# Kernel tuning notes

Hardware: AMD Instinct MI355X
Metric: run time of the kernel (lower is better)

Reference implementation:

```python
import jax, jax.numpy as jnp
import numpy as np

N_SLOW = 26
N_FAST = 12


def _ema(x, N):
    # x: [B, T, F]; standard EMA with alpha = 2/(N+1), initialized y_0 = x_0.
    alpha = jnp.asarray(2.0 / (N + 1), dtype=x.dtype)
    one_m = jnp.asarray(1.0, dtype=x.dtype) - alpha
    xt = jnp.moveaxis(x, 1, 0)  # [T, B, F] for scan over time

    def step(carry, xi):
        y = alpha * xi + one_m * carry
        return y, y

    y0 = xt[0]
    _, ys = jax.lax.scan(step, y0, xt[1:])
    ys = jnp.concatenate([y0[None], ys], axis=0)  # [T, B, F]
    return jnp.moveaxis(ys, 0, 1)  # [B, T, F]


def setup_inputs() -> dict:
    key = jax.random.key(0)
    x = jax.random.normal(key, (4096, 2048, 8), dtype=jnp.float32)
    return {"x": x}


def reference(x):
    # MACD_RNN.forward: EMA_slow(x) - EMA_fast(x)
    return _ema(x, N_SLOW) - _ema(x, N_FAST)
```

## Files before the change

kernel.cpp:

```cpp
#include <hip/hip_runtime.h>


#define T_LEN 2048
#define FDIM 8
#define CHUNK 4
#define NTHR 512
#define NWAVE (NTHR / 64)
#define NF4 (T_LEN * FDIM / 4)
#define SLOTS_PER_CHUNK (CHUNK * FDIM / 4)

__device__ __forceinline__ float pow4(float v) {
    float v2 = v * v;
    return v2 * v2;
}

__device__ __forceinline__ int swz(int g) { return g ^ ((g >> 4) & 7); }

__global__ __launch_bounds__(NTHR, 4)
void macd_kernel(const float* __restrict__ x, float* __restrict__ out) {
    const float AS  = (float)(2.0 / 27.0);
    const float AF  = (float)(2.0 / 13.0);
    const float OMS = 1.0f - AS;
    const float OMF = 1.0f - AF;
    const float DS  = pow4(OMS);
    const float DF  = pow4(OMF);

    __shared__ float4 xb4[NF4];
    __shared__ float  W[NWAVE][16];

    const int b = blockIdx.x;
    const int j = threadIdx.x;
    const int w = j >> 6;
    const int l = j & 63;

    const float4* xg = reinterpret_cast<const float4*>(x   + (size_t)b * T_LEN * FDIM);
    float4*       og = reinterpret_cast<float4*>      (out + (size_t)b * T_LEN * FDIM);

#pragma unroll
    for (int k = 0; k < NF4 / NTHR; ++k) {
        int g = k * NTHR + j;
        xb4[swz(g)] = xg[g];
    }
    __syncthreads();

    const int c   = j;
    const int base = SLOTS_PER_CHUNK * c;
    const int key  = (c >> 1) & 7;
    float p[16];
#pragma unroll
    for (int s = 0; s < 16; ++s) p[s] = 0.f;

#pragma unroll
    for (int t = 0; t < CHUNK; ++t) {
        float4 lo = xb4[base + ((2 * t    ) ^ key)];
        float4 hi = xb4[base + ((2 * t + 1) ^ key)];
        float xx[FDIM] = {lo.x, lo.y, lo.z, lo.w, hi.x, hi.y, hi.z, hi.w};
#pragma unroll
        for (int f = 0; f < FDIM; ++f) {
            p[2 * f + 0] = AS * xx[f] + OMS * p[2 * f + 0];
            p[2 * f + 1] = AF * xx[f] + OMF * p[2 * f + 1];
        }
    }

    const float* xs = reinterpret_cast<const float*>(xb4);
    if (j == 0) {
#pragma unroll
        for (int f = 0; f < FDIM; ++f) {
            float x0 = xs[f];
            p[2 * f + 0] += DS * x0;
            p[2 * f + 1] += DF * x0;
        }
    }

    float Ms = DS, Mf = DF;
#pragma unroll
    for (int off = 1; off < 64; off <<= 1) {
#pragma unroll
        for (int s = 0; s < 16; ++s) {
            float tv = __shfl_up(p[s], (unsigned)off, 64);
            if (l >= off) p[s] += ((s & 1) ? Mf : Ms) * tv;
        }
        Ms *= Ms; Mf *= Mf;
    }

    float qe[16];
#pragma unroll
    for (int s = 0; s < 16; ++s) qe[s] = __shfl_up(p[s], 1u, 64);

    if (l == 63) {
#pragma unroll
        for (int s = 0; s < 16; ++s) W[w][s] = p[s];
    }
    __syncthreads();

    float Sp[16];
#pragma unroll
    for (int s = 0; s < 16; ++s) Sp[s] = 0.f;
    for (int v = 0; v < w; ++v) {
#pragma unroll
        for (int s = 0; s < 16; ++s)
            Sp[s] = W[v][s] + ((s & 1) ? Mf : Ms) * Sp[s];
    }

    float Dls = 1.f, Dlf = 1.f, ms2 = DS, mf2 = DF;
#pragma unroll
    for (int bit = 0; bit < 6; ++bit) {
        if ((l >> bit) & 1) { Dls *= ms2; Dlf *= mf2; }
        ms2 *= ms2; mf2 *= mf2;
    }

    float ys[FDIM], yf[FDIM];
#pragma unroll
    for (int f = 0; f < FDIM; ++f) {
        float cs = (l == 0) ? Sp[2 * f + 0] : qe[2 * f + 0] + Dls * Sp[2 * f + 0];
        float cf = (l == 0) ? Sp[2 * f + 1] : qe[2 * f + 1] + Dlf * Sp[2 * f + 1];
        ys[f] = cs; yf[f] = cf;
    }
    if (j == 0) {
#pragma unroll
        for (int f = 0; f < FDIM; ++f) { ys[f] = xs[f]; yf[f] = xs[f]; }
    }

#pragma unroll
    for (int t = 0; t < CHUNK; ++t) {
        int slo = base + ((2 * t    ) ^ key);
        int shi = base + ((2 * t + 1) ^ key);
        float4 lo = xb4[slo];
        float4 hi = xb4[shi];
        float xx[FDIM] = {lo.x, lo.y, lo.z, lo.w, hi.x, hi.y, hi.z, hi.w};
        float o[FDIM];
#pragma unroll
        for (int f = 0; f < FDIM; ++f) {
            ys[f] = AS * xx[f] + OMS * ys[f];
            yf[f] = AF * xx[f] + OMF * yf[f];
            o[f] = ys[f] - yf[f];
        }
        float4 olo = {o[0], o[1], o[2], o[3]};
        float4 ohi = {o[4], o[5], o[6], o[7]};
        xb4[slo] = olo;
        xb4[shi] = ohi;
    }
    __syncthreads();

#pragma unroll
    for (int k = 0; k < NF4 / NTHR; ++k) {
        int g = k * NTHR + j;
        og[g] = xb4[swz(g)];
    }
}

extern "C" void kernel_launch(void* const* d_in, const int* in_sizes, int n_in,
                              void* d_out, int out_size, void* d_ws, size_t ws_size,
                              hipStream_t stream) {
    (void)n_in; (void)d_ws; (void)ws_size; (void)out_size;
    const float* x = (const float*)d_in[0];
    float* out = (float*)d_out;
    const int B = in_sizes[0] / (T_LEN * FDIM);
    macd_kernel<<<dim3(B), dim3(NTHR), 0, stream>>>(x, out);
}
```

Before: 110.7 us.

## Use persistent blocks with register prefetch and double-buffered LDS

```diff
diff --git a/kernel.cpp b/kernel.cpp
--- a/kernel.cpp
+++ b/kernel.cpp
@@ -2,150 +2,166 @@
 
 
 #define T_LEN 2048
-#define FDIM 8
+#define FDIM  8
 #define CHUNK 4
-#define NTHR 512
+#define NTHR  512
 #define NWAVE (NTHR / 64)
-#define NF4 (T_LEN * FDIM / 4)
-#define SLOTS_PER_CHUNK (CHUNK * FDIM / 4)
-
-__device__ __forceinline__ float pow4(float v) {
-    float v2 = v * v;
-    return v2 * v2;
-}
+#define NF4   (T_LEN * FDIM / 4)
+#define LD_PT (NF4 / NTHR)
+#define GRID  256
 
 __device__ __forceinline__ int swz(int g) { return g ^ ((g >> 4) & 7); }
 
-__global__ __launch_bounds__(NTHR, 4)
-void macd_kernel(const float* __restrict__ x, float* __restrict__ out) {
-    const float AS  = (float)(2.0 / 27.0);
-    const float AF  = (float)(2.0 / 13.0);
+__device__ __forceinline__ void ldsbar() {
+    asm volatile("s_waitcnt lgkmcnt(0)" ::: "memory");
+    __builtin_amdgcn_s_barrier();
+}
+
+__global__ __launch_bounds__(NTHR, 2)
+void macd_kernel(const float* __restrict__ x, float* __restrict__ out, int B) {
+    const float AS  = 2.0f / 27.0f;
+    const float AF  = 2.0f / 13.0f;
     const float OMS = 1.0f - AS;
     const float OMF = 1.0f - AF;
-    const float DS  = pow4(OMS);
-    const float DF  = pow4(OMF);
+    const float DS  = (OMS*OMS)*(OMS*OMS);
+    const float DF  = (OMF*OMF)*(OMF*OMF);
 
-    __shared__ float4 xb4[NF4];
+    __shared__ float4 buf[2][NF4];
     __shared__ float  W[NWAVE][16];
 
-    const int b = blockIdx.x;
     const int j = threadIdx.x;
-    const int w = j >> 6;
-    const int l = j & 63;
+    const int w = j >> 6, l = j & 63;
+    const int c = j;
+    const int base = 8 * c;
+    const int key  = (c >> 1) & 7;
 
-    const float4* xg = reinterpret_cast<const float4*>(x   + (size_t)b * T_LEN * FDIM);
-    float4*       og = reinterpret_cast<float4*>      (out + (size_t)b * T_LEN * FDIM);
-
+    float Dls = 1.f, Dlf = 1.f;
+    {
+        float ms2 = DS, mf2 = DF;
 #pragma unroll
-    for (int k = 0; k < NF4 / NTHR; ++k) {
-        int g = k * NTHR + j;
-        xb4[swz(g)] = xg[g];
-    }
-    __syncthreads();
-
-    const int c   = j;
-    const int base = SLOTS_PER_CHUNK * c;
-    const int key  = (c >> 1) & 7;
-    float p[16];
-#pragma unroll
-    for (int s = 0; s < 16; ++s) p[s] = 0.f;
-
-#pragma unroll
-    for (int t = 0; t < CHUNK; ++t) {
-        float4 lo = xb4[base + ((2 * t    ) ^ key)];
-        float4 hi = xb4[base + ((2 * t + 1) ^ key)];
-        float xx[FDIM] = {lo.x, lo.y, lo.z, lo.w, hi.x, hi.y, hi.z, hi.w};
-#pragma unroll
-        for (int f = 0; f < FDIM; ++f) {
-            p[2 * f + 0] = AS * xx[f] + OMS * p[2 * f + 0];
-            p[2 * f + 1] = AF * xx[f] + OMF * p[2 * f + 1];
+        for (int bit = 0; bit < 6; ++bit) {
+            if ((l >> bit) & 1) { Dls *= ms2; Dlf *= mf2; }
+            ms2 *= ms2; mf2 *= mf2;
         }
     }
 
-    const float* xs = reinterpret_cast<const float*>(xb4);
-    if (j == 0) {
+    int r = blockIdx.x;
+    if (r >= B) return;
+
+    {
+        const float4* xg = (const float4*)(x + (size_t)r * (T_LEN * FDIM));
 #pragma unroll
-        for (int f = 0; f < FDIM; ++f) {
-            float x0 = xs[f];
-            p[2 * f + 0] += DS * x0;
-            p[2 * f + 1] += DF * x0;
+        for (int k = 0; k < LD_PT; ++k) {
+            int g = k * NTHR + j;
+            buf[0][swz(g)] = xg[g];
         }
+        ldsbar();
     }
 
-    float Ms = DS, Mf = DF;
+    int cur = 0;
+    for (; r < B; r += GRID, cur ^= 1) {
+        const int rn = r + GRID;
+        const bool pf = (rn < B);
+        float4 nx[LD_PT];
+        if (pf) {
+            const float4* xg = (const float4*)(x + (size_t)rn * (T_LEN * FDIM));
 #pragma unroll
-    for (int off = 1; off < 64; off <<= 1) {
+            for (int k = 0; k < LD_PT; ++k) nx[k] = xg[k * NTHR + j];
+        }
+
+        float p[16];
 #pragma unroll
-        for (int s = 0; s < 16; ++s) {
-            float tv = __shfl_up(p[s], (unsigned)off, 64);
-            if (l >= off) p[s] += ((s & 1) ? Mf : Ms) * tv;
+        for (int s = 0; s < 16; ++s) p[s] = 0.f;
+#pragma unroll
+        for (int t = 0; t < CHUNK; ++t) {
+            float4 lo = buf[cur][(base + 2*t    ) ^ key];
+            float4 hi = buf[cur][(base + 2*t + 1) ^ key];
+            float xx[8] = {lo.x,lo.y,lo.z,lo.w, hi.x,hi.y,hi.z,hi.w};
+#pragma unroll
+            for (int f = 0; f < 8; ++f) {
+                p[2*f+0] = AS * xx[f] + OMS * p[2*f+0];
+                p[2*f+1] = AF * xx[f] + OMF * p[2*f+1];
+            }
         }
-        Ms *= Ms; Mf *= Mf;
-    }
+        const float* xs = (const float*)&buf[cur][0];
+        if (j == 0) {
+#pragma unroll
+            for (int f = 0; f < 8; ++f) {
+                float x0 = xs[f];
+                p[2*f+0] += DS * x0;
+                p[2*f+1] += DF * x0;
+            }
+        }
 
-    float qe[16];
+        float Ms = DS, Mf = DF;
 #pragma unroll
-    for (int s = 0; s < 16; ++s) qe[s] = __shfl_up(p[s], 1u, 64);
+        for (int off = 1; off < 64; off <<= 1) {
+#pragma unroll
+            for (int s = 0; s < 16; ++s) {
+                float tv = __shfl_up(p[s], (unsigned)off, 64);
+                if (l >= off) p[s] += ((s & 1) ? Mf : Ms) * tv;
+            }
+            Ms *= Ms; Mf *= Mf;
+        }
+        float qe[16];
+#pragma unroll
+        for (int s = 0; s < 16; ++s) qe[s] = __shfl_up(p[s], 1u, 64);
 
-    if (l == 63) {
+        if (l == 63) {
 #pragma unroll
-        for (int s = 0; s < 16; ++s) W[w][s] = p[s];
-    }
-    __syncthreads();
+            for (int s = 0; s < 16; ++s) W[w][s] = p[s];
+        }
+        ldsbar();
+        float Sp[16];
+#pragma unroll
+        for (int s = 0; s < 16; ++s) Sp[s] = 0.f;
+        for (int v = 0; v < w; ++v) {
+#pragma unroll
+            for (int s = 0; s < 16; ++s)
+                Sp[s] = W[v][s] + ((s & 1) ? Mf : Ms) * Sp[s];
+        }
 
-    float Sp[16];
+        float ys[8], yf[8];
 #pragma unroll
-    for (int s = 0; s < 16; ++s) Sp[s] = 0.f;
-    for (int v = 0; v < w; ++v) {
+        for (int f = 0; f < 8; ++f) {
+            ys[f] = (l == 0) ? Sp[2*f+0] : qe[2*f+0] + Dls * Sp[2*f+0];
+            yf[f] = (l == 0) ? Sp[2*f+1] : qe[2*f+1] + Dlf * Sp[2*f+1];
+        }
+        if (j == 0) {
 #pragma unroll
-        for (int s = 0; s < 16; ++s)
-            Sp[s] = W[v][s] + ((s & 1) ? Mf : Ms) * Sp[s];
-    }
+            for (int f = 0; f < 8; ++f) { ys[f] = xs[f]; yf[f] = xs[f]; }
+        }
+#pragma unroll
+        for (int t = 0; t < CHUNK; ++t) {
+            int slo = (base + 2*t    ) ^ key;
+            int shi = (base + 2*t + 1) ^ key;
+            float4 lo = buf[cur][slo];
+            float4 hi = buf[cur][shi];
+            float xx[8] = {lo.x,lo.y,lo.z,lo.w, hi.x,hi.y,hi.z,hi.w};
+            float o[8];
+#pragma unroll
+            for (int f = 0; f < 8; ++f) {
+                ys[f] = AS * xx[f] + OMS * ys[f];
+                yf[f] = AF * xx[f] + OMF * yf[f];
+                o[f]  = ys[f] - yf[f];
+            }
+            buf[cur][slo] = make_float4(o[0], o[1], o[2], o[3]);
+            buf[cur][shi] = make_float4(o[4], o[5], o[6], o[7]);
+        }
+        ldsbar();
 
-    float Dls = 1.f, Dlf = 1.f, ms2 = DS, mf2 = DF;
+        float4* og = (float4*)(out + (size_t)r * (T_LEN * FDIM));
 #pragma unroll
-    for (int bit = 0; bit < 6; ++bit) {
-        if ((l >> bit) & 1) { Dls *= ms2; Dlf *= mf2; }
-        ms2 *= ms2; mf2 *= mf2;
-    }
-
-    float ys[FDIM], yf[FDIM];
+        for (int k = 0; k < LD_PT; ++k) {
+            int g = k * NTHR + j;
+            og[g] = buf[cur][swz(g)];
+        }
+        if (pf) {
 #pragma unroll
-    for (int f = 0; f < FDIM; ++f) {
-        float cs = (l == 0) ? Sp[2 * f + 0] : qe[2 * f + 0] + Dls * Sp[2 * f + 0];
-        float cf = (l == 0) ? Sp[2 * f + 1] : qe[2 * f + 1] + Dlf * Sp[2 * f + 1];
-        ys[f] = cs; yf[f] = cf;
-    }
-    if (j == 0) {
-#pragma unroll
-        for (int f = 0; f < FDIM; ++f) { ys[f] = xs[f]; yf[f] = xs[f]; }
-    }
-
-#pragma unroll
-    for (int t = 0; t < CHUNK; ++t) {
-        int slo = base + ((2 * t    ) ^ key);
-        int shi = base + ((2 * t + 1) ^ key);
-        float4 lo = xb4[slo];
-        float4 hi = xb4[shi];
-        float xx[FDIM] = {lo.x, lo.y, lo.z, lo.w, hi.x, hi.y, hi.z, hi.w};
-        float o[FDIM];
-#pragma unroll
-        for (int f = 0; f < FDIM; ++f) {
-            ys[f] = AS * xx[f] + OMS * ys[f];
-            yf[f] = AF * xx[f] + OMF * yf[f];
-            o[f] = ys[f] - yf[f];
+            for (int k = 0; k < LD_PT; ++k)
+                buf[cur ^ 1][swz(k * NTHR + j)] = nx[k];
         }
-        float4 olo = {o[0], o[1], o[2], o[3]};
-        float4 ohi = {o[4], o[5], o[6], o[7]};
-        xb4[slo] = olo;
-        xb4[shi] = ohi;
-    }
-    __syncthreads();
-
-#pragma unroll
-    for (int k = 0; k < NF4 / NTHR; ++k) {
-        int g = k * NTHR + j;
-        og[g] = xb4[swz(g)];
+        ldsbar();
     }
 }
 
@@ -156,5 +172,6 @@
     const float* x = (const float*)d_in[0];
     float* out = (float*)d_out;
     const int B = in_sizes[0] / (T_LEN * FDIM);
-    macd_kernel<<<dim3(B), dim3(NTHR), 0, stream>>>(x, out);
+    const int grid = (B < GRID) ? B : GRID;
+    macd_kernel<<<dim3(grid), dim3(NTHR), 0, stream>>>(x, out, B);
 }
```

New measurement: 185.3 us. 1.67x slower.
